# Performance work log

Hardware: AMD Instinct MI355X
Metric: run time of the kernel (lower is better)

The kernel has to match this reference:

```python
import jax, jax.numpy as jnp
import numpy as np

N_NODES = 50000
N_EDGES = 800000
N_FEAT = 256


def setup_inputs() -> dict:
    key = jax.random.key(0)
    k_h, k_src, k_dst, k_w1, k_w2 = jax.random.split(key, 5)
    h = jax.random.normal(k_h, (N_NODES, N_FEAT), dtype=jnp.float32)
    src = jax.random.randint(k_src, (N_EDGES,), 0, N_NODES, dtype=jnp.int32)
    dst = jax.random.randint(k_dst, (N_EDGES,), 0, N_NODES, dtype=jnp.int32)
    # Kaiming-uniform-ish init like nn.Linear defaults
    b1 = 1.0 / np.sqrt(2 * N_FEAT)
    b2 = 1.0 / np.sqrt(N_FEAT)
    W1_w = jax.random.uniform(k_w1, (N_FEAT, 2 * N_FEAT), dtype=jnp.float32, minval=-b1, maxval=b1)
    W1_b = jnp.zeros((N_FEAT,), dtype=jnp.float32)
    W2_w = jax.random.uniform(k_w2, (1, N_FEAT), dtype=jnp.float32, minval=-b2, maxval=b2)
    W2_b = jnp.zeros((1,), dtype=jnp.float32)
    return {"h": h, "src": src, "dst": dst, "W1_w": W1_w, "W1_b": W1_b, "W2_w": W2_w, "W2_b": W2_b}


def reference(h, src, dst, W1_w, W1_b, W2_w, W2_b):
    # Gather per-edge endpoint features and concat along feature dim: [E, 2F]
    e = jnp.concatenate([h[src], h[dst]], axis=-1)
    # 2-layer MLP: Linear -> ReLU -> Linear, squeeze to per-edge score [E]
    hid = jax.nn.relu(e @ W1_w.T + W1_b)          # [E, F]
    score = (hid @ W2_w.T + W2_b)[:, 0]            # [E]
    return score
```

## Files before the change

### kernel.cpp

```cpp
#include <hip/hip_runtime.h>

#define F 256
#define TWO_F 512
#define BM 128
#define BN 64
#define BK 64

typedef __attribute__((ext_vector_type(8))) short short8;
typedef __attribute__((ext_vector_type(4))) float float4v;

static __device__ __forceinline__ unsigned short f2bf(float f) {
    unsigned u = __float_as_uint(f);
    u += 0x7FFFu + ((u >> 16) & 1u);
    return (unsigned short)(u >> 16);
}
static __device__ __forceinline__ unsigned pack2(float lo, float hi) {
    unsigned a = __float_as_uint(lo) + 0x8000u;
    unsigned b = __float_as_uint(hi) + 0x8000u;
    return __builtin_amdgcn_perm(b, a, 0x07060302u);
}
static __device__ __forceinline__ float blo(unsigned u) { return __uint_as_float(u << 16); }
static __device__ __forceinline__ float rawf(unsigned u) { return __uint_as_float(u); }

__global__ __launch_bounds__(256) void prep_kernel(
    const float* __restrict__ h, const float* __restrict__ W1,
    unsigned short* __restrict__ hb, unsigned short* __restrict__ Wb, int M)
{
    int i = blockIdx.x * blockDim.x + threadIdx.x;
    if (i < M * 128) {
        int m = i >> 7;
        int kp = (i & 127) * 2;
        float2 v = *(const float2*)(h + (size_t)m * F + kp);
        unsigned pk = pack2(v.x, v.y);
        int ksw = ((kp & 63) + (m & 7) * 8) & 63;
        *(unsigned*)(hb + (size_t)m * F + (kp & ~63) + ksw) = pk;
    }
    if (i < TWO_F * F) {
        int n = i >> 8;
        int k = i & 255;
        float v = W1[(n & 255) * TWO_F + ((n >> 8) << 8) + k];
        int kin_sw = ((k & 63) + (n & 7) * 8) & 63;
        Wb[n * F + (k & ~63) + kin_sw] = f2bf(v);
    }
}

__global__ __launch_bounds__(256, 4) void gemm_kernel(
    const unsigned short* __restrict__ hb, const unsigned short* __restrict__ Wb,
    const float* __restrict__ b1v, unsigned short* __restrict__ C, int M)
{
    __shared__ unsigned short sA[BM * BK];
    __shared__ unsigned short sB[BN * BK];

    const int ib = blockIdx.x;
    const int r8 = ib & 7;
    const int q  = ib >> 3;
    const int by = q & 7;
    const int bx = (q >> 3) * 8 + r8;
    const int bm = bx * BM;
    if (bm >= M) return;
    const int bn = by * BN;

    const int tid  = threadIdx.x;
    const int lane = tid & 63;
    const int wid  = tid >> 6;
    const int st_r = lane >> 3;
    const int st_k = (lane & 7) * 8;
    const int quad = lane >> 4;
    const int l15  = lane & 15;
    const int rot  = (l15 & 7) * 8;

    float4v acc[2][4];
    #pragma unroll
    for (int i = 0; i < 2; ++i)
        #pragma unroll
        for (int j = 0; j < 4; ++j) acc[i][j] = (float4v)(0.f);

    for (int k0 = 0; k0 < F; k0 += BK) {
        #pragma unroll
        for (int p = 0; p < 4; ++p) {
            int r = wid * 32 + p * 8;
            int am = bm + r + st_r; if (am > M - 1) am = M - 1;
            const unsigned short* ga = hb + (size_t)am * F + k0 + st_k;
            __builtin_amdgcn_global_load_lds(
                (const __attribute__((address_space(1))) unsigned int*)ga,
                (__attribute__((address_space(3))) unsigned int*)&sA[r * BK],
                16, 0, 0);
        }
        #pragma unroll
        for (int p = 0; p < 2; ++p) {
            int r = wid * 16 + p * 8;
            const unsigned short* gb = Wb + (size_t)(bn + r + st_r) * F + k0 + st_k;
            __builtin_amdgcn_global_load_lds(
                (const __attribute__((address_space(1))) unsigned int*)gb,
                (__attribute__((address_space(3))) unsigned int*)&sB[r * BK],
                16, 0, 0);
        }
        __syncthreads();

        #pragma unroll
        for (int ks = 0; ks < 2; ++ks) {
            const int koff = (ks * 32 + quad * 8 + rot) & 63;
            short8 afr[2], bfr[4];
            #pragma unroll
            for (int mt = 0; mt < 2; ++mt)
                afr[mt] = *(const short8*)&sA[(wid * 32 + mt * 16 + l15) * BK + koff];
            #pragma unroll
            for (int nt = 0; nt < 4; ++nt)
                bfr[nt] = *(const short8*)&sB[(nt * 16 + l15) * BK + koff];
            #pragma unroll
            for (int mt = 0; mt < 2; ++mt)
                #pragma unroll
                for (int nt = 0; nt < 4; ++nt)
                    acc[mt][nt] = __builtin_amdgcn_mfma_f32_16x16x32_bf16(
                        afr[mt], bfr[nt], acc[mt][nt], 0, 0, 0);
        }
        __syncthreads();
    }

    float bias[4];
    #pragma unroll
    for (int nt = 0; nt < 4; ++nt) {
        int n = bn + nt * 16 + l15;
        bias[nt] = (n < F) ? b1v[n] : 0.f;
    }
    #pragma unroll
    for (int mt = 0; mt < 2; ++mt) {
        int gm0 = bm + wid * 32 + mt * 16 + quad * 4;
        #pragma unroll
        for (int rr = 0; rr < 4; ++rr) {
            int gm = gm0 + rr;
            if (gm < M) {
                unsigned short* cp = C + (size_t)gm * TWO_F + bn + l15;
                #pragma unroll
                for (int nt = 0; nt < 4; ++nt)
                    cp[nt * 16] = f2bf(acc[mt][nt][rr] + bias[nt]);
            }
        }
    }
}

__global__ __launch_bounds__(256) void edge_kernel(
    const unsigned short* __restrict__ C,
    const int* __restrict__ src, const int* __restrict__ dst,
    const float* __restrict__ w2,
    const float* __restrict__ b2, float* __restrict__ out, int E)
{
    const int lane = threadIdx.x & 31;
    const int g = blockIdx.x * 8 + (threadIdx.x >> 5);
    const int e0 = g * 2;
    if (e0 >= E) return;
    const int s0 = src[e0], d0 = dst[e0];
    const int s1 = src[e0 + 1], d1 = dst[e0 + 1];

    uint4 av0 = *(const uint4*)(C + (size_t)s0 * TWO_F + lane * 8);
    uint4 bv0 = *(const uint4*)(C + (size_t)d0 * TWO_F + F + lane * 8);
    uint4 av1 = *(const uint4*)(C + (size_t)s1 * TWO_F + lane * 8);
    uint4 bv1 = *(const uint4*)(C + (size_t)d1 * TWO_F + F + lane * 8);
    float4 w0 = *(const float4*)(w2 + lane * 8);
    float4 w1 = *(const float4*)(w2 + lane * 8 + 4);

    float sum0, sum1;
    sum0  = w0.x * fmaxf(blo(av0.x) + blo(bv0.x), 0.f);
    sum0 += w0.y * fmaxf(rawf(av0.x) + rawf(bv0.x), 0.f);
    sum0 += w0.z * fmaxf(blo(av0.y) + blo(bv0.y), 0.f);
    sum0 += w0.w * fmaxf(rawf(av0.y) + rawf(bv0.y), 0.f);
    sum0 += w1.x * fmaxf(blo(av0.z) + blo(bv0.z), 0.f);
    sum0 += w1.y * fmaxf(rawf(av0.z) + rawf(bv0.z), 0.f);
    sum0 += w1.z * fmaxf(blo(av0.w) + blo(bv0.w), 0.f);
    sum0 += w1.w * fmaxf(rawf(av0.w) + rawf(bv0.w), 0.f);

    sum1  = w0.x * fmaxf(blo(av1.x) + blo(bv1.x), 0.f);
    sum1 += w0.y * fmaxf(rawf(av1.x) + rawf(bv1.x), 0.f);
    sum1 += w0.z * fmaxf(blo(av1.y) + blo(bv1.y), 0.f);
    sum1 += w0.w * fmaxf(rawf(av1.y) + rawf(bv1.y), 0.f);
    sum1 += w1.x * fmaxf(blo(av1.z) + blo(bv1.z), 0.f);
    sum1 += w1.y * fmaxf(rawf(av1.z) + rawf(bv1.z), 0.f);
    sum1 += w1.z * fmaxf(blo(av1.w) + blo(bv1.w), 0.f);
    sum1 += w1.w * fmaxf(rawf(av1.w) + rawf(bv1.w), 0.f);

    #pragma unroll
    for (int off = 16; off > 0; off >>= 1) {
        sum0 += __shfl_down(sum0, off, 32);
        sum1 += __shfl_down(sum1, off, 32);
    }

    if (lane == 0) {
        float b = b2[0];
        out[e0]     = sum0 + b;
        out[e0 + 1] = sum1 + b;
    }
}

extern "C" void kernel_launch(void* const* d_in, const int* in_sizes, int n_in,
                              void* d_out, int out_size, void* d_ws, size_t ws_size,
                              hipStream_t stream) {
    const float* h    = (const float*)d_in[0];
    const int*   src  = (const int*)d_in[1];
    const int*   dst  = (const int*)d_in[2];
    const float* W1_w = (const float*)d_in[3];
    const float* W1_b = (const float*)d_in[4];
    const float* W2_w = (const float*)d_in[5];
    const float* W2_b = (const float*)d_in[6];
    float* out = (float*)d_out;

    const int M = in_sizes[0] / F;
    const int E = in_sizes[1];

    unsigned short* Wb = (unsigned short*)d_ws;
    unsigned short* hb = (unsigned short*)((char*)d_ws + 512 * 1024);
    unsigned short* C  = (unsigned short*)((char*)d_ws + 512 * 1024 + 26 * 1024 * 1024);

    int prep_threads = M * 128 > TWO_F * F ? M * 128 : TWO_F * F;
    prep_kernel<<<(prep_threads + 255) / 256, 256, 0, stream>>>(h, W1_w, hb, Wb, M);

    int nbx = ((M + BM - 1) / BM + 7) / 8 * 8;
    gemm_kernel<<<nbx * 8, 256, 0, stream>>>(hb, Wb, W1_b, C, M);

    edge_kernel<<<(E / 2 + 7) / 8, 256, 0, stream>>>(C, src, dst, W2_w, W2_b, out, E);
}
```

Baseline: 227.1 us.

## Split edge scoring into two feature-half passes to shrink gather working set

The edge kernel now runs twice, each pass gathering only 128 of the 256 hidden features per endpoint. The first pass writes partial scores and the second adds its half plus the bias. The aim is to halve the random-gather footprint of C per pass so it fits better in cache (L2/MALL). In exchange it adds a second launch, re-reads src/dst, does a read-modify-write of the output, and issues narrower 8-byte loads.

New measurement: 233.1 us. 2.6% more time.

```diff
diff --git a/kernel.cpp b/kernel.cpp
--- a/kernel.cpp
+++ b/kernel.cpp
@@ -139,6 +139,7 @@
     }
 }
 
+template<int PASS>
 __global__ __launch_bounds__(256) void edge_kernel(
     const unsigned short* __restrict__ C,
     const int* __restrict__ src, const int* __restrict__ dst,
@@ -152,31 +153,24 @@
     const int s0 = src[e0], d0 = dst[e0];
     const int s1 = src[e0 + 1], d1 = dst[e0 + 1];
 
-    uint4 av0 = *(const uint4*)(C + (size_t)s0 * TWO_F + lane * 8);
-    uint4 bv0 = *(const uint4*)(C + (size_t)d0 * TWO_F + F + lane * 8);
-    uint4 av1 = *(const uint4*)(C + (size_t)s1 * TWO_F + lane * 8);
-    uint4 bv1 = *(const uint4*)(C + (size_t)d1 * TWO_F + F + lane * 8);
-    float4 w0 = *(const float4*)(w2 + lane * 8);
-    float4 w1 = *(const float4*)(w2 + lane * 8 + 4);
+    constexpr int CO = PASS * 128;
+
+    uint2 av0 = *(const uint2*)(C + (size_t)s0 * TWO_F + CO + lane * 4);
+    uint2 bv0 = *(const uint2*)(C + (size_t)d0 * TWO_F + F + CO + lane * 4);
+    uint2 av1 = *(const uint2*)(C + (size_t)s1 * TWO_F + CO + lane * 4);
+    uint2 bv1 = *(const uint2*)(C + (size_t)d1 * TWO_F + F + CO + lane * 4);
+    float4 w = *(const float4*)(w2 + CO + lane * 4);
 
     float sum0, sum1;
-    sum0  = w0.x * fmaxf(blo(av0.x) + blo(bv0.x), 0.f);
-    sum0 += w0.y * fmaxf(rawf(av0.x) + rawf(bv0.x), 0.f);
-    sum0 += w0.z * fmaxf(blo(av0.y) + blo(bv0.y), 0.f);
-    sum0 += w0.w * fmaxf(rawf(av0.y) + rawf(bv0.y), 0.f);
-    sum0 += w1.x * fmaxf(blo(av0.z) + blo(bv0.z), 0.f);
-    sum0 += w1.y * fmaxf(rawf(av0.z) + rawf(bv0.z), 0.f);
-    sum0 += w1.z * fmaxf(blo(av0.w) + blo(bv0.w), 0.f);
-    sum0 += w1.w * fmaxf(rawf(av0.w) + rawf(bv0.w), 0.f);
-
-    sum1  = w0.x * fmaxf(blo(av1.x) + blo(bv1.x), 0.f);
-    sum1 += w0.y * fmaxf(rawf(av1.x) + rawf(bv1.x), 0.f);
-    sum1 += w0.z * fmaxf(blo(av1.y) + blo(bv1.y), 0.f);
-    sum1 += w0.w * fmaxf(rawf(av1.y) + rawf(bv1.y), 0.f);
-    sum1 += w1.x * fmaxf(blo(av1.z) + blo(bv1.z), 0.f);
-    sum1 += w1.y * fmaxf(rawf(av1.z) + rawf(bv1.z), 0.f);
-    sum1 += w1.z * fmaxf(blo(av1.w) + blo(bv1.w), 0.f);
-    sum1 += w1.w * fmaxf(rawf(av1.w) + rawf(bv1.w), 0.f);
+    sum0  = w.x * fmaxf(blo(av0.x) + blo(bv0.x), 0.f);
+    sum0 += w.y * fmaxf(rawf(av0.x) + rawf(bv0.x), 0.f);
+    sum0 += w.z * fmaxf(blo(av0.y) + blo(bv0.y), 0.f);
+    sum0 += w.w * fmaxf(rawf(av0.y) + rawf(bv0.y), 0.f);
+
+    sum1  = w.x * fmaxf(blo(av1.x) + blo(bv1.x), 0.f);
+    sum1 += w.y * fmaxf(rawf(av1.x) + rawf(bv1.x), 0.f);
+    sum1 += w.z * fmaxf(blo(av1.y) + blo(bv1.y), 0.f);
+    sum1 += w.w * fmaxf(rawf(av1.y) + rawf(bv1.y), 0.f);
 
     #pragma unroll
     for (int off = 16; off > 0; off >>= 1) {
@@ -185,9 +179,14 @@
     }
 
     if (lane == 0) {
-        float b = b2[0];
-        out[e0]     = sum0 + b;
-        out[e0 + 1] = sum1 + b;
+        if (PASS == 0) {
+            out[e0]     = sum0;
+            out[e0 + 1] = sum1;
+        } else {
+            float b = b2[0];
+            out[e0]     = out[e0]     + sum0 + b;
+            out[e0 + 1] = out[e0 + 1] + sum1 + b;
+        }
     }
 }
 
@@ -216,5 +215,7 @@
     int nbx = ((M + BM - 1) / BM + 7) / 8 * 8;
     gemm_kernel<<<nbx * 8, 256, 0, stream>>>(hb, Wb, W1_b, C, M);
 
-    edge_kernel<<<(E / 2 + 7) / 8, 256, 0, stream>>>(C, src, dst, W2_w, W2_b, out, E);
-}
+    int eblocks = (E / 2 + 7) / 8;
+    edge_kernel<0><<<eblocks, 256, 0, stream>>>(C, src, dst, W2_w, W2_b, out, E);
+    edge_kernel<1><<<eblocks, 256, 0, stream>>>(C, src, dst, W2_w, W2_b, out, E);
+}
```
